# Performance work log

Measured on AMD Instinct MI355X. Metric: run time of the kernel, lower is better.

## Reference

```python
import jax, jax.numpy as jnp
import numpy as np

N, D = 16384, 2048


def setup_inputs() -> dict:
    key = jax.random.key(0)
    k1, k2, k3, k4 = jax.random.split(key, 4)
    X = jax.random.normal(k1, (N, D), dtype=jnp.float32)
    keep = jax.random.uniform(k4, (N, D)) > 0.5
    X = jnp.where(keep, X, 0.0)
    A = jax.random.normal(k2, (D, D), dtype=jnp.float32)
    b = jax.random.normal(k3, (D,), dtype=jnp.float32)
    return {"X": X, "A": A, "b": b}


def reference(X, A, b):
    # y_pred = X @ A.T + b
    y_pred = jnp.einsum('nd,kd->nk', X, A) + b  # [N, D]
    mask = X != 0
    masked = jnp.where(mask, y_pred, 0.0)
    row_sum = masked.sum(axis=1, keepdims=True)          # [N, 1]
    has_any = mask.any(axis=1, keepdims=True)            # [N, 1]
    y_out = jnp.where(mask, masked / row_sum, 0.0)
    # rows with an empty mask stay all-zero (matches the Python-loop guard)
    y_out = jnp.where(has_any, y_out, 0.0)
    return y_out
```

## Files before the change

kernel.cpp:

```cpp
#include <hip/hip_runtime.h>

#define N_ROWS 16384
#define D_DIM  2048
#define BM 128
#define BN 128
#define BK 32
#define NKT (D_DIM / BK)

typedef __attribute__((ext_vector_type(8))) _Float16 half8;
typedef __attribute__((ext_vector_type(4))) _Float16 half4_t;
typedef __attribute__((ext_vector_type(4))) float floatx4;

typedef __attribute__((address_space(1))) const unsigned int as1_uint;
typedef __attribute__((address_space(3))) unsigned int as3_uint;

__device__ __forceinline__ void gload_lds16(const _Float16* g, _Float16* l) {
    __builtin_amdgcn_global_load_lds((as1_uint*)g, (as3_uint*)l, 16, 0, 0);
}

__global__ void split_mask_kernel(const float4* __restrict__ src,
                                  half4_t* __restrict__ dh,
                                  half4_t* __restrict__ dl,
                                  unsigned char* __restrict__ mask,
                                  int count8)
{
    for (int i = blockIdx.x * blockDim.x + threadIdx.x; i < count8;
         i += gridDim.x * blockDim.x) {
        float4 a = src[2 * i];
        float4 b = src[2 * i + 1];
        half4_t ha, la, hb, lb;
        ha[0] = (_Float16)a.x; ha[1] = (_Float16)a.y;
        ha[2] = (_Float16)a.z; ha[3] = (_Float16)a.w;
        la[0] = (_Float16)((a.x - (float)ha[0]) * 4096.0f);
        la[1] = (_Float16)((a.y - (float)ha[1]) * 4096.0f);
        la[2] = (_Float16)((a.z - (float)ha[2]) * 4096.0f);
        la[3] = (_Float16)((a.w - (float)ha[3]) * 4096.0f);
        hb[0] = (_Float16)b.x; hb[1] = (_Float16)b.y;
        hb[2] = (_Float16)b.z; hb[3] = (_Float16)b.w;
        lb[0] = (_Float16)((b.x - (float)hb[0]) * 4096.0f);
        lb[1] = (_Float16)((b.y - (float)hb[1]) * 4096.0f);
        lb[2] = (_Float16)((b.z - (float)hb[2]) * 4096.0f);
        lb[3] = (_Float16)((b.w - (float)hb[3]) * 4096.0f);
        dh[2 * i] = ha; dh[2 * i + 1] = hb;
        dl[2 * i] = la; dl[2 * i + 1] = lb;
        unsigned int m = 0;
        m |= (a.x != 0.0f) ? 0x01u : 0u;  m |= (a.y != 0.0f) ? 0x02u : 0u;
        m |= (a.z != 0.0f) ? 0x04u : 0u;  m |= (a.w != 0.0f) ? 0x08u : 0u;
        m |= (b.x != 0.0f) ? 0x10u : 0u;  m |= (b.y != 0.0f) ? 0x20u : 0u;
        m |= (b.z != 0.0f) ? 0x40u : 0u;  m |= (b.w != 0.0f) ? 0x80u : 0u;
        mask[i] = (unsigned char)m;
    }
}

__global__ void split_kernel(const float4* __restrict__ src,
                             half4_t* __restrict__ dh,
                             half4_t* __restrict__ dl, int count4)
{
    for (int i = blockIdx.x * blockDim.x + threadIdx.x; i < count4;
         i += gridDim.x * blockDim.x) {
        float4 v = src[i];
        half4_t h, l;
        h[0] = (_Float16)v.x; h[1] = (_Float16)v.y;
        h[2] = (_Float16)v.z; h[3] = (_Float16)v.w;
        l[0] = (_Float16)((v.x - (float)h[0]) * 4096.0f);
        l[1] = (_Float16)((v.y - (float)h[1]) * 4096.0f);
        l[2] = (_Float16)((v.z - (float)h[2]) * 4096.0f);
        l[3] = (_Float16)((v.w - (float)h[3]) * 4096.0f);
        dh[i] = h; dl[i] = l;
    }
}

__global__ __launch_bounds__(256, 2)
void gemm_presplit_kernel(const _Float16* __restrict__ Xh,
                          const _Float16* __restrict__ Xl,
                          const _Float16* __restrict__ Ah,
                          const _Float16* __restrict__ Al,
                          const unsigned char* __restrict__ maskbits,
                          const float* __restrict__ bias,
                          float* __restrict__ out)
{
    __shared__ __align__(16) _Float16 sXh[2][BM * BK];
    __shared__ __align__(16) _Float16 sXl[2][BM * BK];
    __shared__ __align__(16) _Float16 sAh[2][BN * BK];
    __shared__ __align__(16) _Float16 sAl[2][BN * BK];

    const int t   = threadIdx.x;
    const int bid = blockIdx.x;

    const int xcd    = bid & 7;
    const int local  = bid >> 3;
    const int r_tile = (xcd << 4) + (local & 15);
    const int c_tile = local >> 4;
    const int m0 = r_tile * BM;
    const int n0 = c_tile * BN;

    const int lane  = t & 63;
    const int w     = t >> 6;
    const int wr    = w >> 1;
    const int wc    = w & 1;
    const int lrow  = lane & 15;
    const int lslot = lane >> 4;

    floatx4 acc1[4][4], acc2[4][4];
    #pragma unroll
    for (int mi = 0; mi < 4; ++mi)
        #pragma unroll
        for (int ni = 0; ni < 4; ++ni)
            #pragma unroll
            for (int j = 0; j < 4; ++j) { acc1[mi][ni][j] = 0.f; acc2[mi][ni][j] = 0.f; }

    const _Float16* gsrc;
    _Float16* lb0; _Float16* lb1;
    if      (w == 0) { gsrc = Xh + (size_t)m0 * D_DIM; lb0 = &sXh[0][0]; lb1 = &sXh[1][0]; }
    else if (w == 1) { gsrc = Xl + (size_t)m0 * D_DIM; lb0 = &sXl[0][0]; lb1 = &sXl[1][0]; }
    else if (w == 2) { gsrc = Ah + (size_t)n0 * D_DIM; lb0 = &sAh[0][0]; lb1 = &sAh[1][0]; }
    else             { gsrc = Al + (size_t)n0 * D_DIM; lb0 = &sAl[0][0]; lb1 = &sAl[1][0]; }

    int off8[8];
    #pragma unroll
    for (int i = 0; i < 8; ++i) {
        int c = i * 64 + lane;
        int row = c >> 2;
        int sp  = c & 3;
        int kslot = sp ^ ((row >> 1) & 3);
        off8[i] = row * D_DIM + kslot * 8;
    }

    auto issue = [&](int buf, int kt) {
        _Float16* lb = buf ? lb1 : lb0;
        const _Float16* gk = gsrc + kt * BK;
        #pragma unroll
        for (int i = 0; i < 8; ++i)
            gload_lds16(gk + off8[i], lb + i * 512);
    };

    issue(0, 0);

    int cur = 0;
    for (int kt = 0; kt < NKT; ++kt) {
        __syncthreads();
        if (kt + 1 < NKT) issue(cur ^ 1, kt + 1);

        half8 bhf[4], blf[4];
        #pragma unroll
        for (int ni = 0; ni < 4; ++ni) {
            int row = wc * 64 + ni * 16 + lrow;
            int off = row * BK + ((lslot ^ ((row >> 1) & 3)) << 3);
            bhf[ni] = *reinterpret_cast<const half8*>(&sAh[cur][off]);
            blf[ni] = *reinterpret_cast<const half8*>(&sAl[cur][off]);
        }
        #pragma unroll
        for (int mi = 0; mi < 4; ++mi) {
            int row = wr * 64 + mi * 16 + lrow;
            int off = row * BK + ((lslot ^ ((row >> 1) & 3)) << 3);
            half8 ah = *reinterpret_cast<const half8*>(&sXh[cur][off]);
            half8 al = *reinterpret_cast<const half8*>(&sXl[cur][off]);
            #pragma unroll
            for (int ni = 0; ni < 4; ++ni) {
                acc1[mi][ni] = __builtin_amdgcn_mfma_f32_16x16x32_f16(ah, bhf[ni], acc1[mi][ni], 0, 0, 0);
                acc2[mi][ni] = __builtin_amdgcn_mfma_f32_16x16x32_f16(ah, blf[ni], acc2[mi][ni], 0, 0, 0);
                acc2[mi][ni] = __builtin_amdgcn_mfma_f32_16x16x32_f16(al, bhf[ni], acc2[mi][ni], 0, 0, 0);
            }
        }
        cur ^= 1;
    }

    #pragma unroll
    for (int mi = 0; mi < 4; ++mi) {
        #pragma unroll
        for (int ni = 0; ni < 4; ++ni) {
            int c = n0 + wc * 64 + ni * 16 + lrow;
            float bv = bias[c];
            #pragma unroll
            for (int j = 0; j < 4; ++j) {
                int r = m0 + wr * 64 + mi * 16 + lslot * 4 + j;
                size_t idx = (size_t)r * D_DIM + c;
                float v = acc1[mi][ni][j] + acc2[mi][ni][j] * (1.0f / 4096.0f) + bv;
                unsigned int bit = (maskbits[idx >> 3] >> (c & 7)) & 1u;
                out[idx] = bit ? v : 0.0f;
            }
        }
    }
}

__global__ __launch_bounds__(256, 2)
void gemm_mask_kernel(const float* __restrict__ X,
                      const float* __restrict__ A,
                      const float* __restrict__ bias,
                      float* __restrict__ out)
{
    __shared__ __align__(16) _Float16 sXh[2][BM * BK];
    __shared__ __align__(16) _Float16 sXl[2][BM * BK];
    __shared__ __align__(16) _Float16 sAh[2][BN * BK];
    __shared__ __align__(16) _Float16 sAl[2][BN * BK];

    const int t   = threadIdx.x;
    const int bid = blockIdx.x;
    const int xcd    = bid & 7;
    const int local  = bid >> 3;
    const int r_tile = (xcd << 4) + (local & 15);
    const int c_tile = local >> 4;
    const int m0 = r_tile * BM;
    const int n0 = c_tile * BN;

    const int lane  = t & 63;
    const int w     = t >> 6;
    const int wr    = w >> 1;
    const int wc    = w & 1;
    const int lrow  = lane & 15;
    const int lslot = lane >> 4;

    const float4* X4 = reinterpret_cast<const float4*>(X);
    const float4* A4 = reinterpret_cast<const float4*>(A);

    floatx4 acc1[4][4], acc2[4][4];
    #pragma unroll
    for (int mi = 0; mi < 4; ++mi)
        #pragma unroll
        for (int ni = 0; ni < 4; ++ni)
            #pragma unroll
            for (int j = 0; j < 4; ++j) { acc1[mi][ni][j] = 0.f; acc2[mi][ni][j] = 0.f; }

    float4 rx[4], ra[4];
    #pragma unroll
    for (int i = 0; i < 4; ++i) {
        int f = i * 256 + t; int row = f >> 3; int k4 = f & 7;
        rx[i] = X4[(size_t)(m0 + row) * (D_DIM / 4) + k4];
        ra[i] = A4[(size_t)(n0 + row) * (D_DIM / 4) + k4];
    }

    auto stage = [&](const float4* rv, _Float16* dsh, _Float16* dsl) {
        #pragma unroll
        for (int i = 0; i < 4; ++i) {
            int f = i * 256 + t; int row = f >> 3; int k4 = f & 7;
            float4 v = rv[i];
            half4_t h, l;
            h[0] = (_Float16)v.x; h[1] = (_Float16)v.y;
            h[2] = (_Float16)v.z; h[3] = (_Float16)v.w;
            l[0] = (_Float16)((v.x - (float)h[0]) * 4096.0f);
            l[1] = (_Float16)((v.y - (float)h[1]) * 4096.0f);
            l[2] = (_Float16)((v.z - (float)h[2]) * 4096.0f);
            l[3] = (_Float16)((v.w - (float)h[3]) * 4096.0f);
            int off = row * BK + ((((k4 >> 1) ^ ((row >> 1) & 3)) << 3) + ((k4 & 1) << 2));
            *reinterpret_cast<half4_t*>(dsh + off) = h;
            *reinterpret_cast<half4_t*>(dsl + off) = l;
        }
    };

    stage(rx, &sXh[0][0], &sXl[0][0]);
    stage(ra, &sAh[0][0], &sAl[0][0]);

    int cur = 0;
    for (int kt = 0; kt < NKT; ++kt) {
        __syncthreads();
        const bool more = (kt + 1 < NKT);
        if (more) {
            int kb = (kt + 1) * (BK / 4);
            #pragma unroll
            for (int i = 0; i < 4; ++i) {
                int f = i * 256 + t; int row = f >> 3; int k4 = f & 7;
                rx[i] = X4[(size_t)(m0 + row) * (D_DIM / 4) + kb + k4];
                ra[i] = A4[(size_t)(n0 + row) * (D_DIM / 4) + kb + k4];
            }
        }

        half8 bhf[4], blf[4];
        #pragma unroll
        for (int ni = 0; ni < 4; ++ni) {
            int row = wc * 64 + ni * 16 + lrow;
            int off = row * BK + ((lslot ^ ((row >> 1) & 3)) << 3);
            bhf[ni] = *reinterpret_cast<const half8*>(&sAh[cur][off]);
            blf[ni] = *reinterpret_cast<const half8*>(&sAl[cur][off]);
        }
        #pragma unroll
        for (int mi = 0; mi < 4; ++mi) {
            int row = wr * 64 + mi * 16 + lrow;
            int off = row * BK + ((lslot ^ ((row >> 1) & 3)) << 3);
            half8 ah = *reinterpret_cast<const half8*>(&sXh[cur][off]);
            half8 al = *reinterpret_cast<const half8*>(&sXl[cur][off]);
            #pragma unroll
            for (int ni = 0; ni < 4; ++ni) {
                acc1[mi][ni] = __builtin_amdgcn_mfma_f32_16x16x32_f16(ah, bhf[ni], acc1[mi][ni], 0, 0, 0);
                acc2[mi][ni] = __builtin_amdgcn_mfma_f32_16x16x32_f16(ah, blf[ni], acc2[mi][ni], 0, 0, 0);
                acc2[mi][ni] = __builtin_amdgcn_mfma_f32_16x16x32_f16(al, bhf[ni], acc2[mi][ni], 0, 0, 0);
            }
        }

        if (more) {
            int nxt = cur ^ 1;
            stage(rx, &sXh[nxt][0], &sXl[nxt][0]);
            stage(ra, &sAh[nxt][0], &sAl[nxt][0]);
            cur = nxt;
        }
    }

    #pragma unroll
    for (int mi = 0; mi < 4; ++mi) {
        #pragma unroll
        for (int ni = 0; ni < 4; ++ni) {
            int c = n0 + wc * 64 + ni * 16 + lrow;
            float bv = bias[c];
            #pragma unroll
            for (int j = 0; j < 4; ++j) {
                int r = m0 + wr * 64 + mi * 16 + lslot * 4 + j;
                float v = acc1[mi][ni][j] + acc2[mi][ni][j] * (1.0f / 4096.0f) + bv;
                float xv = X[(size_t)r * D_DIM + c];
                out[(size_t)r * D_DIM + c] = (xv != 0.0f) ? v : 0.0f;
            }
        }
    }
}

__global__ void row_sum_inv_kernel(const float* __restrict__ out, float* __restrict__ inv)
{
    int gw = (blockIdx.x * 256 + threadIdx.x) >> 6;
    int l  = threadIdx.x & 63;
    const float4* row = reinterpret_cast<const float4*>(out) + (size_t)gw * (D_DIM / 4);
    float s = 0.f;
    #pragma unroll
    for (int j = 0; j < 8; ++j) {
        float4 v = row[j * 64 + l];
        s += (v.x + v.y) + (v.z + v.w);
    }
    #pragma unroll
    for (int off = 32; off > 0; off >>= 1) s += __shfl_down(s, off, 64);
    if (l == 0) inv[gw] = (s != 0.0f) ? (1.0f / s) : 0.0f;
}

__global__ void scale_kernel(float* __restrict__ out, const float* __restrict__ inv)
{
    const int total = N_ROWS * (D_DIM / 4);
    float4* o = reinterpret_cast<float4*>(out);
    for (int i = blockIdx.x * blockDim.x + threadIdx.x; i < total;
         i += gridDim.x * blockDim.x) {
        float s  = inv[i >> 9];
        float4 v = o[i];
        v.x *= s; v.y *= s; v.z *= s; v.w *= s;
        o[i] = v;
    }
}

extern "C" void kernel_launch(void* const* d_in, const int* in_sizes, int n_in,
                              void* d_out, int out_size, void* d_ws, size_t ws_size,
                              hipStream_t stream)
{
    const float* X  = (const float*)d_in[0];
    const float* A  = (const float*)d_in[1];
    const float* b  = (const float*)d_in[2];
    float* out = (float*)d_out;

    const size_t nX = (size_t)N_ROWS * D_DIM;
    const size_t nA = (size_t)D_DIM * D_DIM;
    const size_t inv_bytes  = (size_t)N_ROWS * sizeof(float);
    const size_t mask_bytes = nX / 8;
    const size_t need = inv_bytes + 2 * nX * 2 + 2 * nA * 2 + mask_bytes;

    if (ws_size >= need) {
        float*         inv = (float*)d_ws;
        _Float16*      Xh  = (_Float16*)((char*)d_ws + inv_bytes);
        _Float16*      Xl  = Xh + nX;
        _Float16*      Ah  = Xl + nX;
        _Float16*      Al  = Ah + nA;
        unsigned char* mb  = (unsigned char*)(Al + nA);

        hipLaunchKernelGGL(split_mask_kernel, dim3(4096), dim3(256), 0, stream,
                           (const float4*)X, (half4_t*)Xh, (half4_t*)Xl, mb, (int)(nX / 8));
        hipLaunchKernelGGL(split_kernel, dim3(1024), dim3(256), 0, stream,
                           (const float4*)A, (half4_t*)Ah, (half4_t*)Al, (int)(nA / 4));
        hipLaunchKernelGGL(gemm_presplit_kernel, dim3((N_ROWS / BM) * (D_DIM / BN)), dim3(256), 0, stream,
                           Xh, Xl, Ah, Al, mb, b, out);
        hipLaunchKernelGGL(row_sum_inv_kernel, dim3(N_ROWS / 4), dim3(256), 0, stream, out, inv);
        hipLaunchKernelGGL(scale_kernel, dim3(2048), dim3(256), 0, stream, out, inv);
    } else {
        float* inv = (float*)d_ws;
        hipLaunchKernelGGL(gemm_mask_kernel, dim3((N_ROWS / BM) * (D_DIM / BN)), dim3(256), 0, stream,
                           X, A, b, out);
        hipLaunchKernelGGL(row_sum_inv_kernel, dim3(N_ROWS / 4), dim3(256), 0, stream, out, inv);
        hipLaunchKernelGGL(scale_kernel, dim3(2048), dim3(256), 0, stream, out, inv);
    }
}
```

Baseline: 496.3 us.

## Use 32x32 MFMA tiles and fuse masked row-sum partials into GEMM epilogue

Switches the split-precision GEMM from 16x16x32 to 32x32x16 MFMA instructions, which cuts LDS fragment reads per FLOP. The epilogue also computes per-row partial sums of the masked output, reduced with wavefront shuffles, and writes them to a small workspace buffer. A new lightweight kernel reduces those partials to inverse row sums, replacing the row_sum_inv pass that re-read the full output. The cost is a larger workspace, extra shuffles and register pressure in the epilogue, and a less coalesced store pattern for the 32x32 accumulator layout.

Result: slower. 517.1 us (+4.2%).

```diff
diff --git a/kernel.cpp b/kernel.cpp
--- a/kernel.cpp
+++ b/kernel.cpp
@@ -7,9 +7,10 @@
 #define BK 32
 #define NKT (D_DIM / BK)
 
-typedef __attribute__((ext_vector_type(8))) _Float16 half8;
-typedef __attribute__((ext_vector_type(4))) _Float16 half4_t;
-typedef __attribute__((ext_vector_type(4))) float floatx4;
+typedef __attribute__((ext_vector_type(8)))  _Float16 half8;
+typedef __attribute__((ext_vector_type(4)))  _Float16 half4_t;
+typedef __attribute__((ext_vector_type(4)))  float floatx4;
+typedef __attribute__((ext_vector_type(16))) float floatx16;
 
 typedef __attribute__((address_space(1))) const unsigned int as1_uint;
 typedef __attribute__((address_space(3))) unsigned int as3_uint;
@@ -71,13 +72,14 @@
 }
 
 __global__ __launch_bounds__(256, 2)
-void gemm_presplit_kernel(const _Float16* __restrict__ Xh,
-                          const _Float16* __restrict__ Xl,
-                          const _Float16* __restrict__ Ah,
-                          const _Float16* __restrict__ Al,
-                          const unsigned char* __restrict__ maskbits,
-                          const float* __restrict__ bias,
-                          float* __restrict__ out)
+void gemm_presplit32_kernel(const _Float16* __restrict__ Xh,
+                            const _Float16* __restrict__ Xl,
+                            const _Float16* __restrict__ Ah,
+                            const _Float16* __restrict__ Al,
+                            const unsigned char* __restrict__ maskbits,
+                            const float* __restrict__ bias,
+                            float* __restrict__ out,
+                            float* __restrict__ partials)
 {
     __shared__ __align__(16) _Float16 sXh[2][BM * BK];
     __shared__ __align__(16) _Float16 sXl[2][BM * BK];
@@ -94,20 +96,20 @@
     const int m0 = r_tile * BM;
     const int n0 = c_tile * BN;
 
-    const int lane  = t & 63;
-    const int w     = t >> 6;
-    const int wr    = w >> 1;
-    const int wc    = w & 1;
-    const int lrow  = lane & 15;
-    const int lslot = lane >> 4;
-
-    floatx4 acc1[4][4], acc2[4][4];
-    #pragma unroll
-    for (int mi = 0; mi < 4; ++mi)
-        #pragma unroll
-        for (int ni = 0; ni < 4; ++ni)
-            #pragma unroll
-            for (int j = 0; j < 4; ++j) { acc1[mi][ni][j] = 0.f; acc2[mi][ni][j] = 0.f; }
+    const int lane = t & 63;
+    const int w    = t >> 6;
+    const int wr   = w >> 1;
+    const int wc   = w & 1;
+    const int l31  = lane & 31;
+    const int hi5  = lane >> 5;
+
+    floatx16 acc1[2][2], acc2[2][2];
+    #pragma unroll
+    for (int mi = 0; mi < 2; ++mi)
+        #pragma unroll
+        for (int ni = 0; ni < 2; ++ni)
+            #pragma unroll
+            for (int q = 0; q < 16; ++q) { acc1[mi][ni][q] = 0.f; acc2[mi][ni][q] = 0.f; }
 
     const _Float16* gsrc;
     _Float16* lb0; _Float16* lb1;
@@ -141,46 +143,89 @@
         __syncthreads();
         if (kt + 1 < NKT) issue(cur ^ 1, kt + 1);
 
-        half8 bhf[4], blf[4];
-        #pragma unroll
-        for (int ni = 0; ni < 4; ++ni) {
-            int row = wc * 64 + ni * 16 + lrow;
-            int off = row * BK + ((lslot ^ ((row >> 1) & 3)) << 3);
-            bhf[ni] = *reinterpret_cast<const half8*>(&sAh[cur][off]);
-            blf[ni] = *reinterpret_cast<const half8*>(&sAl[cur][off]);
-        }
-        #pragma unroll
-        for (int mi = 0; mi < 4; ++mi) {
-            int row = wr * 64 + mi * 16 + lrow;
-            int off = row * BK + ((lslot ^ ((row >> 1) & 3)) << 3);
-            half8 ah = *reinterpret_cast<const half8*>(&sXh[cur][off]);
-            half8 al = *reinterpret_cast<const half8*>(&sXl[cur][off]);
-            #pragma unroll
-            for (int ni = 0; ni < 4; ++ni) {
-                acc1[mi][ni] = __builtin_amdgcn_mfma_f32_16x16x32_f16(ah, bhf[ni], acc1[mi][ni], 0, 0, 0);
-                acc2[mi][ni] = __builtin_amdgcn_mfma_f32_16x16x32_f16(ah, blf[ni], acc2[mi][ni], 0, 0, 0);
-                acc2[mi][ni] = __builtin_amdgcn_mfma_f32_16x16x32_f16(al, bhf[ni], acc2[mi][ni], 0, 0, 0);
-            }
+        half8 bh[2][2], bl[2][2];
+        #pragma unroll
+        for (int ni = 0; ni < 2; ++ni)
+            #pragma unroll
+            for (int kk = 0; kk < 2; ++kk) {
+                int row = wc * 64 + ni * 32 + l31;
+                int s   = kk * 2 + hi5;
+                int off = row * BK + ((s ^ ((row >> 1) & 3)) << 3);
+                bh[ni][kk] = *reinterpret_cast<const half8*>(&sAh[cur][off]);
+                bl[ni][kk] = *reinterpret_cast<const half8*>(&sAl[cur][off]);
+            }
+        #pragma unroll
+        for (int mi = 0; mi < 2; ++mi) {
+            half8 ah[2], al[2];
+            #pragma unroll
+            for (int kk = 0; kk < 2; ++kk) {
+                int row = wr * 64 + mi * 32 + l31;
+                int s   = kk * 2 + hi5;
+                int off = row * BK + ((s ^ ((row >> 1) & 3)) << 3);
+                ah[kk] = *reinterpret_cast<const half8*>(&sXh[cur][off]);
+                al[kk] = *reinterpret_cast<const half8*>(&sXl[cur][off]);
+            }
+            #pragma unroll
+            for (int ni = 0; ni < 2; ++ni)
+                #pragma unroll
+                for (int kk = 0; kk < 2; ++kk) {
+                    acc1[mi][ni] = __builtin_amdgcn_mfma_f32_32x32x16_f16(ah[kk], bh[ni][kk], acc1[mi][ni], 0, 0, 0);
+                    acc2[mi][ni] = __builtin_amdgcn_mfma_f32_32x32x16_f16(ah[kk], bl[ni][kk], acc2[mi][ni], 0, 0, 0);
+                    acc2[mi][ni] = __builtin_amdgcn_mfma_f32_32x32x16_f16(al[kk], bh[ni][kk], acc2[mi][ni], 0, 0, 0);
+                }
         }
         cur ^= 1;
     }
 
     #pragma unroll
-    for (int mi = 0; mi < 4; ++mi) {
-        #pragma unroll
-        for (int ni = 0; ni < 4; ++ni) {
-            int c = n0 + wc * 64 + ni * 16 + lrow;
+    for (int mi = 0; mi < 2; ++mi) {
+        float rs[16];
+        #pragma unroll
+        for (int q = 0; q < 16; ++q) rs[q] = 0.f;
+        #pragma unroll
+        for (int ni = 0; ni < 2; ++ni) {
+            int c = n0 + wc * 64 + ni * 32 + l31;
             float bv = bias[c];
             #pragma unroll
-            for (int j = 0; j < 4; ++j) {
-                int r = m0 + wr * 64 + mi * 16 + lslot * 4 + j;
+            for (int q = 0; q < 16; ++q) {
+                int rrow = (q & 3) + 8 * (q >> 2) + 4 * hi5;
+                int r = m0 + wr * 64 + mi * 32 + rrow;
                 size_t idx = (size_t)r * D_DIM + c;
-                float v = acc1[mi][ni][j] + acc2[mi][ni][j] * (1.0f / 4096.0f) + bv;
+                float v = acc1[mi][ni][q] + acc2[mi][ni][q] * (1.0f / 4096.0f) + bv;
                 unsigned int bit = (maskbits[idx >> 3] >> (c & 7)) & 1u;
-                out[idx] = bit ? v : 0.0f;
-            }
-        }
-    }
+                float mv = bit ? v : 0.0f;
+                out[idx] = mv;
+                rs[q] += mv;
+            }
+        }
+        #pragma unroll
+        for (int q = 0; q < 16; ++q) {
+            float s = rs[q];
+            s += __shfl_xor(s, 1, 64);
+            s += __shfl_xor(s, 2, 64);
+            s += __shfl_xor(s, 4, 64);
+            s += __shfl_xor(s, 8, 64);
+            s += __shfl_xor(s, 16, 64);
+            if (l31 == 0) {
+                int rrow = (q & 3) + 8 * (q >> 2) + 4 * hi5;
+                int r = m0 + wr * 64 + mi * 32 + rrow;
+                partials[(size_t)r * 32 + c_tile * 2 + wc] = s;
+            }
+        }
+    }
+}
+
+__global__ void partial_inv_kernel(const float4* __restrict__ p4, float* __restrict__ inv)
+{
+    int gid  = blockIdx.x * 256 + threadIdx.x;
+    int r    = gid >> 3;
+    int slot = gid & 7;
+    float4 v = p4[(size_t)r * 8 + slot];
+    float s = (v.x + v.y) + (v.z + v.w);
+    s += __shfl_xor(s, 1, 64);
+    s += __shfl_xor(s, 2, 64);
+    s += __shfl_xor(s, 4, 64);
+    if (slot == 0) inv[r] = (s != 0.0f) ? (1.0f / s) : 0.0f;
 }
 
 __global__ __launch_bounds__(256, 2)
@@ -352,24 +397,27 @@
     const size_t nX = (size_t)N_ROWS * D_DIM;
     const size_t nA = (size_t)D_DIM * D_DIM;
     const size_t inv_bytes  = (size_t)N_ROWS * sizeof(float);
+    const size_t part_bytes = (size_t)N_ROWS * 32 * sizeof(float);
     const size_t mask_bytes = nX / 8;
-    const size_t need = inv_bytes + 2 * nX * 2 + 2 * nA * 2 + mask_bytes;
+    const size_t need = inv_bytes + part_bytes + 2 * nX * 2 + 2 * nA * 2 + mask_bytes;
 
     if (ws_size >= need) {
-        float*         inv = (float*)d_ws;
-        _Float16*      Xh  = (_Float16*)((char*)d_ws + inv_bytes);
-        _Float16*      Xl  = Xh + nX;
-        _Float16*      Ah  = Xl + nX;
-        _Float16*      Al  = Ah + nA;
-        unsigned char* mb  = (unsigned char*)(Al + nA);
+        float*         inv  = (float*)d_ws;
+        float*         part = (float*)((char*)d_ws + inv_bytes);
+        _Float16*      Xh   = (_Float16*)((char*)d_ws + inv_bytes + part_bytes);
+        _Float16*      Xl   = Xh + nX;
+        _Float16*      Ah   = Xl + nX;
+        _Float16*      Al   = Ah + nA;
+        unsigned char* mb   = (unsigned char*)(Al + nA);
 
         hipLaunchKernelGGL(split_mask_kernel, dim3(4096), dim3(256), 0, stream,
                            (const float4*)X, (half4_t*)Xh, (half4_t*)Xl, mb, (int)(nX / 8));
         hipLaunchKernelGGL(split_kernel, dim3(1024), dim3(256), 0, stream,
                            (const float4*)A, (half4_t*)Ah, (half4_t*)Al, (int)(nA / 4));
-        hipLaunchKernelGGL(gemm_presplit_kernel, dim3((N_ROWS / BM) * (D_DIM / BN)), dim3(256), 0, stream,
-                           Xh, Xl, Ah, Al, mb, b, out);
-        hipLaunchKernelGGL(row_sum_inv_kernel, dim3(N_ROWS / 4), dim3(256), 0, stream, out, inv);
+        hipLaunchKernelGGL(gemm_presplit32_kernel, dim3((N_ROWS / BM) * (D_DIM / BN)), dim3(256), 0, stream,
+                           Xh, Xl, Ah, Al, mb, b, out, part);
+        hipLaunchKernelGGL(partial_inv_kernel, dim3(N_ROWS * 8 / 256), dim3(256), 0, stream,
+                           (const float4*)part, inv);
         hipLaunchKernelGGL(scale_kernel, dim3(2048), dim3(256), 0, stream, out, inv);
     } else {
         float* inv = (float*)d_ws;
```

## Fuse masked row-sum partials into GEMM epilogue and remap tile order

Applied to the files above, without the earlier changes.

The GEMM epilogue now accumulates masked row sums per wave, reduces them across lanes with shuffles, and writes per-tile partial sums to a workspace buffer. A small kernel combines the 32 partials per row into an inverse, replacing the separate pass that re-read the full 128 MB output. The block-to-tile mapping is also swapped so each XCD walks column tiles within a row band instead of row tiles within a column, which changes L2 reuse of X versus A. This adds a workspace and a few shuffles to the epilogue.

Result: no change. 505.3 us (+1.8%).

```diff
diff --git a/kernel.cpp b/kernel.cpp
--- a/kernel.cpp
+++ b/kernel.cpp
@@ -7,9 +7,9 @@
 #define BK 32
 #define NKT (D_DIM / BK)
 
-typedef __attribute__((ext_vector_type(8))) _Float16 half8;
-typedef __attribute__((ext_vector_type(4))) _Float16 half4_t;
-typedef __attribute__((ext_vector_type(4))) float floatx4;
+typedef __attribute__((ext_vector_type(8)))  _Float16 half8;
+typedef __attribute__((ext_vector_type(4)))  _Float16 half4_t;
+typedef __attribute__((ext_vector_type(4)))  float floatx4;
 
 typedef __attribute__((address_space(1))) const unsigned int as1_uint;
 typedef __attribute__((address_space(3))) unsigned int as3_uint;
@@ -77,7 +77,8 @@
                           const _Float16* __restrict__ Al,
                           const unsigned char* __restrict__ maskbits,
                           const float* __restrict__ bias,
-                          float* __restrict__ out)
+                          float* __restrict__ out,
+                          float* __restrict__ partials)
 {
     __shared__ __align__(16) _Float16 sXh[2][BM * BK];
     __shared__ __align__(16) _Float16 sXl[2][BM * BK];
@@ -89,8 +90,8 @@
 
     const int xcd    = bid & 7;
     const int local  = bid >> 3;
-    const int r_tile = (xcd << 4) + (local & 15);
-    const int c_tile = local >> 4;
+    const int r_tile = (xcd << 4) + (local >> 4);
+    const int c_tile = local & 15;
     const int m0 = r_tile * BM;
     const int n0 = c_tile * BN;
 
@@ -167,6 +168,9 @@
 
     #pragma unroll
     for (int mi = 0; mi < 4; ++mi) {
+        float rs[4];
+        #pragma unroll
+        for (int j = 0; j < 4; ++j) rs[j] = 0.f;
         #pragma unroll
         for (int ni = 0; ni < 4; ++ni) {
             int c = n0 + wc * 64 + ni * 16 + lrow;
@@ -177,10 +181,37 @@
                 size_t idx = (size_t)r * D_DIM + c;
                 float v = acc1[mi][ni][j] + acc2[mi][ni][j] * (1.0f / 4096.0f) + bv;
                 unsigned int bit = (maskbits[idx >> 3] >> (c & 7)) & 1u;
-                out[idx] = bit ? v : 0.0f;
-            }
-        }
-    }
+                float mv = bit ? v : 0.0f;
+                out[idx] = mv;
+                rs[j] += mv;
+            }
+        }
+        #pragma unroll
+        for (int j = 0; j < 4; ++j) {
+            float s = rs[j];
+            s += __shfl_xor(s, 1, 64);
+            s += __shfl_xor(s, 2, 64);
+            s += __shfl_xor(s, 4, 64);
+            s += __shfl_xor(s, 8, 64);
+            if (lrow == 0) {
+                int r = m0 + wr * 64 + mi * 16 + lslot * 4 + j;
+                partials[(size_t)r * 32 + c_tile * 2 + wc] = s;
+            }
+        }
+    }
+}
+
+__global__ void partial_inv_kernel(const float4* __restrict__ p4, float* __restrict__ inv)
+{
+    int gid  = blockIdx.x * 256 + threadIdx.x;
+    int r    = gid >> 3;
+    int slot = gid & 7;
+    float4 v = p4[(size_t)r * 8 + slot];
+    float s = (v.x + v.y) + (v.z + v.w);
+    s += __shfl_xor(s, 1, 64);
+    s += __shfl_xor(s, 2, 64);
+    s += __shfl_xor(s, 4, 64);
+    if (slot == 0) inv[r] = (s != 0.0f) ? (1.0f / s) : 0.0f;
 }
 
 __global__ __launch_bounds__(256, 2)
@@ -352,24 +383,27 @@
     const size_t nX = (size_t)N_ROWS * D_DIM;
     const size_t nA = (size_t)D_DIM * D_DIM;
     const size_t inv_bytes  = (size_t)N_ROWS * sizeof(float);
+    const size_t part_bytes = (size_t)N_ROWS * 32 * sizeof(float);
     const size_t mask_bytes = nX / 8;
-    const size_t need = inv_bytes + 2 * nX * 2 + 2 * nA * 2 + mask_bytes;
+    const size_t need = inv_bytes + part_bytes + 2 * nX * 2 + 2 * nA * 2 + mask_bytes;
 
     if (ws_size >= need) {
-        float*         inv = (float*)d_ws;
-        _Float16*      Xh  = (_Float16*)((char*)d_ws + inv_bytes);
-        _Float16*      Xl  = Xh + nX;
-        _Float16*      Ah  = Xl + nX;
-        _Float16*      Al  = Ah + nA;
-        unsigned char* mb  = (unsigned char*)(Al + nA);
+        float*         inv  = (float*)d_ws;
+        float*         part = (float*)((char*)d_ws + inv_bytes);
+        _Float16*      Xh   = (_Float16*)((char*)d_ws + inv_bytes + part_bytes);
+        _Float16*      Xl   = Xh + nX;
+        _Float16*      Ah   = Xl + nX;
+        _Float16*      Al   = Ah + nA;
+        unsigned char* mb   = (unsigned char*)(Al + nA);
 
         hipLaunchKernelGGL(split_mask_kernel, dim3(4096), dim3(256), 0, stream,
                            (const float4*)X, (half4_t*)Xh, (half4_t*)Xl, mb, (int)(nX / 8));
         hipLaunchKernelGGL(split_kernel, dim3(1024), dim3(256), 0, stream,
                            (const float4*)A, (half4_t*)Ah, (half4_t*)Al, (int)(nA / 4));
         hipLaunchKernelGGL(gemm_presplit_kernel, dim3((N_ROWS / BM) * (D_DIM / BN)), dim3(256), 0, stream,
-                           Xh, Xl, Ah, Al, mb, b, out);
-        hipLaunchKernelGGL(row_sum_inv_kernel, dim3(N_ROWS / 4), dim3(256), 0, stream, out, inv);
+                           Xh, Xl, Ah, Al, mb, b, out, part);
+        hipLaunchKernelGGL(partial_inv_kernel, dim3(N_ROWS * 8 / 256), dim3(256), 0, stream,
+                           (const float4*)part, inv);
         hipLaunchKernelGGL(scale_kernel, dim3(2048), dim3(256), 0, stream, out, inv);
     } else {
         float* inv = (float*)d_ws;
```
